# Performance work log

Hardware: AMD Instinct MI355X
Metric: run time of the kernel (lower is better)

## Reference

```python
import jax, jax.numpy as jnp
import numpy as np

N_NODES = 50000
N_EDGES = 800000
C_IN = 64
C_OUT = 64
C_MSG = C_IN + 3 + 3 + 1  # 71: feat + coords + pos-diff + dist
NUM_TYPES = 2


def setup_inputs() -> dict:
    key = jax.random.key(0)
    k0, k1, k2, k3, k4, k5 = jax.random.split(key, 6)
    input_feature = jax.random.normal(k0, (N_NODES, C_IN), dtype=jnp.float32)
    pos = jax.random.uniform(k1, (N_NODES, 3), dtype=jnp.float32)
    edge_index = jax.random.randint(k2, (2, N_EDGES), 0, N_NODES, dtype=jnp.int32)
    edge_attr = jax.random.randint(k3, (N_EDGES,), 0, NUM_TYPES, dtype=jnp.int32)
    W = jax.random.normal(k4, (NUM_TYPES, C_MSG, C_OUT), dtype=jnp.float32) / np.sqrt(C_MSG)
    b = jax.random.normal(k5, (NUM_TYPES, C_OUT), dtype=jnp.float32) * 0.01
    return {"input_feature": input_feature, "pos": pos, "W": W, "b": b,
            "edge_index": edge_index, "edge_attr": edge_attr}


def reference(input_feature, pos, W, b, edge_index, edge_attr):
    # MyConv.forward: concat node coords (graph.x[..., :3]) onto features
    x = jnp.concatenate([input_feature, pos], axis=-1)  # [N, C_IN+3]
    src = edge_index[0]  # j (source)
    dst = edge_index[1]  # i (target, aggregation index)

    x_j = x[src]                               # [E, C_IN+3]
    diff = pos[dst] - pos[src]                 # x_i[...,-3:] - x_j[...,-3:], [E, 3]
    abs_dist = jnp.linalg.norm(diff, axis=1, keepdims=True)  # [E, 1]
    msg_in = jnp.concatenate([x_j, diff, abs_dist], axis=-1)  # [E, C_MSG]

    # HeteroLinear with 2 types: compute both GEMMs, select per edge type
    y0 = msg_in @ W[0] + b[0]
    y1 = msg_in @ W[1] + b[1]
    msg = jnp.where((edge_attr == 1)[:, None], y1, y0)  # [E, C_OUT]

    # aggr='max' scatter into target nodes; empty segments -> 0 (torch_scatter fill)
    out = jax.ops.segment_max(msg, dst, num_segments=N_NODES)
    out = jnp.where(jnp.isfinite(out), out, jnp.zeros((), out.dtype))
    return out
```

## Files before the change

### kernel.cpp

```cpp
#include <hip/hip_runtime.h>
#include <math.h>

#define NNODES 50000
#define NEDGES 800000
#define COUT 64
#define TILE_E 64
#define NTILES (NEDGES / TILE_E)
#define GRID 1024
#define KEY_NEG_INF 0x007FFFFFu
#define NB1 391
#define NB1P 392
#define CHUNK 2048
#define P2CAP 2816

typedef short bf16x8 __attribute__((ext_vector_type(8)));
typedef float f32x4 __attribute__((ext_vector_type(4)));
#define MFMA16 __builtin_amdgcn_mfma_f32_16x16x32_bf16

__device__ __forceinline__ unsigned short f2bf(float x) {
    union { float f; unsigned u; } v; v.f = x;
    unsigned r = v.u + 0x7fffu + ((v.u >> 16) & 1u);
    return (unsigned short)(r >> 16);
}

__device__ __forceinline__ unsigned fkey(float v) {
    unsigned u = __float_as_uint(v);
    return u ^ ((unsigned)((int)u >> 31) | 0x80000000u);
}

__global__ void prep_kernel(const float* __restrict__ feat, unsigned short* __restrict__ featbf,
                            unsigned* __restrict__ out) {
    int i = blockIdx.x * blockDim.x + threadIdx.x;
    int st = gridDim.x * blockDim.x;
    for (int j = i; j < (NNODES * COUT) / 8; j += st) {
        const float4* pp = (const float4*)(feat + (size_t)j * 8);
        float4 x = pp[0], y = pp[1];
        union { unsigned short u[8]; uint4 v; } r;
        r.u[0] = f2bf(x.x); r.u[1] = f2bf(x.y); r.u[2] = f2bf(x.z); r.u[3] = f2bf(x.w);
        r.u[4] = f2bf(y.x); r.u[5] = f2bf(y.y); r.u[6] = f2bf(y.z); r.u[7] = f2bf(y.w);
        ((uint4*)featbf)[j] = r.v;
    }
    for (int j = i; j < NNODES * COUT; j += st) out[j] = KEY_NEG_INF;
}

__global__ __launch_bounds__(256) void p1a_kernel(const int* __restrict__ ei,
                                                  unsigned* __restrict__ cnt1) {
    __shared__ unsigned h[NB1];
    const int t = threadIdx.x, blk = blockIdx.x;
    for (int i = t; i < NB1; i += 256) h[i] = 0u;
    __syncthreads();
    const int e0 = blk * CHUNK;
    for (int i = t; i < CHUNK; i += 256) {
        int e = e0 + i;
        if (e < NEDGES) atomicAdd(&h[(unsigned)ei[NEDGES + e] >> 7], 1u);
    }
    __syncthreads();
    for (int i = t; i < NB1; i += 256) cnt1[blk * NB1P + i] = h[i];
}

__global__ __launch_bounds__(512) void p1b_kernel(const unsigned* __restrict__ cnt1,
                                                  unsigned* __restrict__ off0,
                                                  unsigned* __restrict__ totals) {
    __shared__ unsigned sh[512];
    const int t = threadIdx.x, b = blockIdx.x;
    unsigned v = (t < NB1) ? cnt1[t * NB1P + b] : 0u;
    sh[t] = v;
    __syncthreads();
    for (int off = 1; off < 512; off <<= 1) {
        unsigned add = (t >= off) ? sh[t - off] : 0u;
        __syncthreads();
        sh[t] += add;
        __syncthreads();
    }
    if (t < NB1) off0[t * NB1P + b] = sh[t] - v;
    if (t == 511) totals[b] = sh[511];
}

__global__ __launch_bounds__(512) void p1c_kernel(const unsigned* __restrict__ totals,
                                                  unsigned* __restrict__ base) {
    __shared__ unsigned sh[512];
    const int t = threadIdx.x;
    unsigned v = (t < NB1) ? totals[t] : 0u;
    sh[t] = v;
    __syncthreads();
    for (int off = 1; off < 512; off <<= 1) {
        unsigned add = (t >= off) ? sh[t - off] : 0u;
        __syncthreads();
        sh[t] += add;
        __syncthreads();
    }
    if (t <= NB1) base[t] = sh[t] - v;
}

__global__ __launch_bounds__(256) void p1d_kernel(const int* __restrict__ ei,
                                                  const int* __restrict__ ea,
                                                  const unsigned* __restrict__ off0,
                                                  const unsigned* __restrict__ base,
                                                  int2* __restrict__ rec) {
    __shared__ unsigned h[NB1];
    const int t = threadIdx.x, blk = blockIdx.x;
    for (int i = t; i < NB1; i += 256) h[i] = 0u;
    __syncthreads();
    const int e0 = blk * CHUNK;
    for (int i = t; i < CHUNK; i += 256) {
        int e = e0 + i;
        if (e < NEDGES) {
            int d = ei[NEDGES + e];
            unsigned b = (unsigned)d >> 7;
            unsigned rk = atomicAdd(&h[b], 1u);
            unsigned pos = base[b] + off0[blk * NB1P + b] + rk;
            rec[pos] = make_int2(ei[e] | (ea[e] << 20), d);
        }
    }
}

__global__ __launch_bounds__(512) void p2_kernel(const unsigned* __restrict__ base,
                                                 int2* __restrict__ rec) {
    __shared__ int2 buf[P2CAP];
    __shared__ unsigned hist[128], dbase[128];
    const int t = threadIdx.x, b = blockIdx.x;
    const unsigned lo = base[b];
    int n = (int)(base[b + 1] - lo);
    if (n > P2CAP) n = P2CAP;
    for (int i = t; i < 128; i += 512) hist[i] = 0u;
    __syncthreads();
    for (int i = t; i < n; i += 512) {
        int2 r = rec[lo + i];
        buf[i] = r;
        atomicAdd(&hist[r.y & 127], 1u);
    }
    __syncthreads();
    if (t < 64) {
        unsigned h0 = hist[2 * t], h1 = hist[2 * t + 1];
        unsigned s = h0 + h1;
        unsigned inc = s;
        #pragma unroll
        for (int off = 1; off < 64; off <<= 1) {
            unsigned nb = __shfl_up(inc, off, 64);
            if (t >= off) inc += nb;
        }
        unsigned excl = inc - s;
        dbase[2 * t] = excl;
        dbase[2 * t + 1] = excl + h0;
    }
    __syncthreads();
    for (int i = t; i < 128; i += 512) hist[i] = 0u;
    __syncthreads();
    for (int i = t; i < n; i += 512) {
        int2 r = buf[i];
        int ld = r.y & 127;
        unsigned rk = atomicAdd(&hist[ld], 1u);
        rec[lo + dbase[ld] + rk] = r;
    }
}

__global__ void finalize_kernel(float* __restrict__ out, int n) {
    int i = blockIdx.x * blockDim.x + threadIdx.x;
    int stride = gridDim.x * blockDim.x;
    for (; i < n; i += stride) {
        unsigned k = ((unsigned*)out)[i];
        unsigned u = (k & 0x80000000u) ? (k ^ 0x80000000u) : ~k;
        out[i] = (u == 0xFF800000u) ? 0.0f : __uint_as_float(u);
    }
}

__global__ __launch_bounds__(256, 4) void edge_mfma_kernel(
    const unsigned short* __restrict__ featbf, const float* __restrict__ pos,
    const float* __restrict__ W, const float* __restrict__ b,
    const int2* __restrict__ rec, unsigned* __restrict__ out)
{
    __shared__ char SMEM[37376];
    bf16x8*   Amsg = (bf16x8*)SMEM;
    unsigned* Kt   = (unsigned*)(SMEM + 20480);
    int*      dstv = (int*)(SMEM + 36864);

    const int tid = threadIdx.x;
    const int lane = tid & 63, w = tid >> 6;
    const int rg = w >> 1, cg = w & 1;
    const int la = lane & 15, lh = lane >> 4;
    const bf16x8 zero8 = {0, 0, 0, 0, 0, 0, 0, 0};

    {
        unsigned short* Ws = (unsigned short*)SMEM;
        for (int idx = tid; idx < 160 * 64; idx += 256) {
            int k = idx >> 6, j = idx & 63;
            int t = (k >= 80);
            int kk = k - t * 80;
            float v = 0.0f;
            if (kk < 71)       v = W[(t * 71 + kk) * 64 + j];
            else if (kk == 71) v = b[t * 64 + j];
            Ws[j * 160 + k] = f2bf(v);
        }
    }
    __syncthreads();
    bf16x8 wb0[5], wb1[5];
    {
        const bf16x8* Wv = (const bf16x8*)SMEM;
        const int c0 = cg * 32 + la, c1 = c0 + 16;
        #pragma unroll
        for (int ks = 0; ks < 5; ++ks) {
            wb0[ks] = Wv[c0 * 20 + ks * 4 + lh];
            wb1[ks] = Wv[c1 * 20 + ks * 4 + lh];
        }
    }
    __syncthreads();
    if (tid < 128) {
        Amsg[(9 + (tid >> 6) * 10) * 64 + (tid & 63)] = zero8;
    }
    __syncthreads();

    const int row = tid >> 2, c = tid & 3;

    int it = 0;
    for (int tile = blockIdx.x; tile < NTILES; tile += GRID, ++it) {
        const int p = it & 1;
        const int2 r2 = rec[tile * TILE_E + row];
        const int src = r2.x & 0xFFFFF;
        const int t = r2.x >> 20;
        const int ot = 1 - t;

        const uint4* g = (const uint4*)(featbf + (size_t)src * 64);
        uint4 q0 = g[2 * c], q1 = g[2 * c + 1];
        *(uint4*)&Amsg[(t * 10 + 2 * c) * 64 + row]     = q0;
        *(uint4*)&Amsg[(t * 10 + 2 * c + 1) * 64 + row] = q1;
        Amsg[(ot * 10 + 2 * c) * 64 + row]     = zero8;
        Amsg[(ot * 10 + 2 * c + 1) * 64 + row] = zero8;

        if (c == 0) {
            int dst = r2.y;
            float ps0 = pos[src * 3], ps1 = pos[src * 3 + 1], ps2 = pos[src * 3 + 2];
            float d0 = pos[dst * 3] - ps0, d1 = pos[dst * 3 + 1] - ps1, d2 = pos[dst * 3 + 2] - ps2;
            float dist = sqrtf(d0 * d0 + d1 * d1 + d2 * d2);
            union { bf16x8 v; unsigned short u[8]; } pt;
            pt.u[0] = f2bf(ps0); pt.u[1] = f2bf(ps1); pt.u[2] = f2bf(ps2);
            pt.u[3] = f2bf(d0);  pt.u[4] = f2bf(d1);  pt.u[5] = f2bf(d2);
            pt.u[6] = f2bf(dist); pt.u[7] = f2bf(1.0f);
            Amsg[(t * 10 + 8) * 64 + row] = pt.v;
        } else if (c == 1) {
            Amsg[(ot * 10 + 8) * 64 + row] = zero8;
        } else if (c == 3) {
            dstv[p * 64 + row] = r2.y;
        }
        __syncthreads();

        f32x4 acc00 = {0,0,0,0}, acc01 = {0,0,0,0}, acc10 = {0,0,0,0}, acc11 = {0,0,0,0};
        const int r0 = rg * 32 + la, r1 = r0 + 16;
        #pragma unroll
        for (int ks = 0; ks < 5; ++ks) {
            bf16x8 a0 = Amsg[(ks * 4 + lh) * 64 + r0];
            bf16x8 a1 = Amsg[(ks * 4 + lh) * 64 + r1];
            acc00 = MFMA16(a0, wb0[ks], acc00, 0, 0, 0);
            acc01 = MFMA16(a0, wb1[ks], acc01, 0, 0, 0);
            acc10 = MFMA16(a1, wb0[ks], acc10, 0, 0, 0);
            acc11 = MFMA16(a1, wb1[ks], acc11, 0, 0, 0);
        }

        const int col0 = cg * 32 + la, col1 = col0 + 16;
        #pragma unroll
        for (int i = 0; i < 4; ++i) {
            int e0 = rg * 32 + lh * 4 + i, e1 = e0 + 16;
            Kt[e0 * 64 + (col0 ^ ((e0 << 2) & 31))] = fkey(acc00[i]);
            Kt[e0 * 64 + (col1 ^ ((e0 << 2) & 31))] = fkey(acc01[i]);
            Kt[e1 * 64 + (col0 ^ ((e1 << 2) & 31))] = fkey(acc10[i]);
            Kt[e1 * 64 + (col1 ^ ((e1 << 2) & 31))] = fkey(acc11[i]);
        }
        __syncthreads();

        {
            const int colr = tid & 63;
            const int rbeg = (tid >> 6) * 16;
            unsigned cur = Kt[rbeg * 64 + (colr ^ ((rbeg << 2) & 31))];
            int curd = dstv[p * 64 + rbeg];
            #pragma unroll
            for (int r = rbeg + 1; r < rbeg + 16; ++r) {
                unsigned k = Kt[r * 64 + (colr ^ ((r << 2) & 31))];
                int d = dstv[p * 64 + r];
                if (d != curd) {
                    atomicMax(out + (size_t)curd * COUT + colr, cur);
                    curd = d; cur = k;
                } else {
                    cur = (k > cur) ? k : cur;
                }
            }
            atomicMax(out + (size_t)curd * COUT + colr, cur);
        }
    }
}

extern "C" void kernel_launch(void* const* d_in, const int* in_sizes, int n_in,
                              void* d_out, int out_size, void* d_ws, size_t ws_size,
                              hipStream_t stream) {
    const float* feat = (const float*)d_in[0];
    const float* pos  = (const float*)d_in[1];
    const float* W    = (const float*)d_in[2];
    const float* b    = (const float*)d_in[3];
    const int*   ei   = (const int*)d_in[4];
    const int*   ea   = (const int*)d_in[5];
    unsigned* out = (unsigned*)d_out;

    unsigned short* featbf = (unsigned short*)d_ws;
    int2*     rec    = (int2*)((char*)d_ws + (size_t)NNODES * COUT * 2);
    unsigned* cnt1   = (unsigned*)(rec + NEDGES);
    unsigned* off0   = cnt1 + NB1 * NB1P;
    unsigned* totals = off0 + NB1 * NB1P;
    unsigned* base   = totals + NB1P;

    prep_kernel<<<2048, 256, 0, stream>>>(feat, featbf, out);
    p1a_kernel<<<NB1, 256, 0, stream>>>(ei, cnt1);
    p1b_kernel<<<NB1, 512, 0, stream>>>(cnt1, off0, totals);
    p1c_kernel<<<1, 512, 0, stream>>>(totals, base);
    p1d_kernel<<<NB1, 256, 0, stream>>>(ei, ea, off0, base, rec);
    p2_kernel<<<NB1, 512, 0, stream>>>(base, rec);
    edge_mfma_kernel<<<GRID, 256, 0, stream>>>(featbf, pos, W, b, rec, out);
    finalize_kernel<<<2048, 256, 0, stream>>>((float*)out, NNODES * COUT);
}
```

Before: 176.4 us.

## Flush max-reduction directly from MFMA accumulators, drop LDS transpose, raise occupancy

Removes the LDS key-transpose buffer and its extra barrier. Each lane now run-length reduces its 4 accumulator rows per column pair and issues atomicMax straight from registers. This shrinks shared memory enough to raise launch bounds to 7 blocks per CU and the grid to 1792. The trade-off is more global atomics, because runs are only merged across 4 rows instead of 16. The single dstv buffer now relies on the trailing barrier before the next tile overwrites it.

```diff
diff --git a/kernel.cpp b/kernel.cpp
--- a/kernel.cpp
+++ b/kernel.cpp
@@ -6,7 +6,7 @@
 #define COUT 64
 #define TILE_E 64
 #define NTILES (NEDGES / TILE_E)
-#define GRID 1024
+#define GRID 1792
 #define KEY_NEG_INF 0x007FFFFFu
 #define NB1 391
 #define NB1P 392
@@ -164,15 +164,37 @@
     }
 }
 
-__global__ __launch_bounds__(256, 4) void edge_mfma_kernel(
+__device__ __forceinline__ void flush4x2(const f32x4& a, const f32x4& bq, int R,
+                                         const int* __restrict__ dv,
+                                         int col0, int col1,
+                                         unsigned* __restrict__ out) {
+    int curd = dv[R];
+    unsigned ca = fkey(a[0]), cb = fkey(bq[0]);
+    #pragma unroll
+    for (int j = 1; j < 4; ++j) {
+        int d = dv[R + j];
+        unsigned ka = fkey(a[j]), kb = fkey(bq[j]);
+        if (d == curd) {
+            ca = (ka > ca) ? ka : ca;
+            cb = (kb > cb) ? kb : cb;
+        } else {
+            atomicMax(out + (size_t)curd * COUT + col0, ca);
+            atomicMax(out + (size_t)curd * COUT + col1, cb);
+            curd = d; ca = ka; cb = kb;
+        }
+    }
+    atomicMax(out + (size_t)curd * COUT + col0, ca);
+    atomicMax(out + (size_t)curd * COUT + col1, cb);
+}
+
+__global__ __launch_bounds__(256, 7) void edge_mfma_kernel(
     const unsigned short* __restrict__ featbf, const float* __restrict__ pos,
     const float* __restrict__ W, const float* __restrict__ b,
     const int2* __restrict__ rec, unsigned* __restrict__ out)
 {
-    __shared__ char SMEM[37376];
-    bf16x8*   Amsg = (bf16x8*)SMEM;
-    unsigned* Kt   = (unsigned*)(SMEM + 20480);
-    int*      dstv = (int*)(SMEM + 36864);
+    __shared__ char SMEM[20736];
+    bf16x8* Amsg = (bf16x8*)SMEM;
+    int*    dstv = (int*)(SMEM + 20480);
 
     const int tid = threadIdx.x;
     const int lane = tid & 63, w = tid >> 6;
@@ -211,9 +233,7 @@
 
     const int row = tid >> 2, c = tid & 3;
 
-    int it = 0;
-    for (int tile = blockIdx.x; tile < NTILES; tile += GRID, ++it) {
-        const int p = it & 1;
+    for (int tile = blockIdx.x; tile < NTILES; tile += GRID) {
         const int2 r2 = rec[tile * TILE_E + row];
         const int src = r2.x & 0xFFFFF;
         const int t = r2.x >> 20;
@@ -239,7 +259,7 @@
         } else if (c == 1) {
             Amsg[(ot * 10 + 8) * 64 + row] = zero8;
         } else if (c == 3) {
-            dstv[p * 64 + row] = r2.y;
+            dstv[row] = r2.y;
         }
         __syncthreads();
 
@@ -255,35 +275,13 @@
             acc11 = MFMA16(a1, wb1[ks], acc11, 0, 0, 0);
         }
 
-        const int col0 = cg * 32 + la, col1 = col0 + 16;
-        #pragma unroll
-        for (int i = 0; i < 4; ++i) {
-            int e0 = rg * 32 + lh * 4 + i, e1 = e0 + 16;
-            Kt[e0 * 64 + (col0 ^ ((e0 << 2) & 31))] = fkey(acc00[i]);
-            Kt[e0 * 64 + (col1 ^ ((e0 << 2) & 31))] = fkey(acc01[i]);
-            Kt[e1 * 64 + (col0 ^ ((e1 << 2) & 31))] = fkey(acc10[i]);
-            Kt[e1 * 64 + (col1 ^ ((e1 << 2) & 31))] = fkey(acc11[i]);
-        }
-        __syncthreads();
-
         {
-            const int colr = tid & 63;
-            const int rbeg = (tid >> 6) * 16;
-            unsigned cur = Kt[rbeg * 64 + (colr ^ ((rbeg << 2) & 31))];
-            int curd = dstv[p * 64 + rbeg];
-            #pragma unroll
-            for (int r = rbeg + 1; r < rbeg + 16; ++r) {
-                unsigned k = Kt[r * 64 + (colr ^ ((r << 2) & 31))];
-                int d = dstv[p * 64 + r];
-                if (d != curd) {
-                    atomicMax(out + (size_t)curd * COUT + colr, cur);
-                    curd = d; cur = k;
-                } else {
-                    cur = (k > cur) ? k : cur;
-                }
-            }
-            atomicMax(out + (size_t)curd * COUT + colr, cur);
-        }
+            const int col0 = cg * 32 + la, col1 = col0 + 16;
+            const int R0 = rg * 32 + lh * 4;
+            flush4x2(acc00, acc01, R0,      dstv, col0, col1, out);
+            flush4x2(acc10, acc11, R0 + 16, dstv, col0, col1, out);
+        }
+        __syncthreads();
     }
 }
 
```

Result: slower. 269.6 us (+52.8%).

## Software-pipeline edge gathers across tiles and use barriers without a vmem wait

Applied to the files above, without the earlier changes.

Prefetches the next tile's edge record, source features and position values into registers while the current tile runs its MFMA and atomic scatter phases. The two __syncthreads calls are replaced by a custom barrier that waits only on LDS counters, so outstanding global loads stay in flight across barriers. The aim is to hide gather latency behind compute and atomics, at the cost of extra registers that may lower occupancy under the 4-wave launch bound.

```diff
diff --git a/kernel.cpp b/kernel.cpp
--- a/kernel.cpp
+++ b/kernel.cpp
@@ -28,6 +28,13 @@
     return u ^ ((unsigned)((int)u >> 31) | 0x80000000u);
 }
 
+__device__ __forceinline__ void soft_barrier() {
+    __builtin_amdgcn_sched_barrier(0);
+    asm volatile("s_waitcnt lgkmcnt(0)" ::: "memory");
+    __builtin_amdgcn_s_barrier();
+    __builtin_amdgcn_sched_barrier(0);
+}
+
 __global__ void prep_kernel(const float* __restrict__ feat, unsigned short* __restrict__ featbf,
                             unsigned* __restrict__ out) {
     int i = blockIdx.x * blockDim.x + threadIdx.x;
@@ -179,6 +186,21 @@
     const int rg = w >> 1, cg = w & 1;
     const int la = lane & 15, lh = lane >> 4;
     const bf16x8 zero8 = {0, 0, 0, 0, 0, 0, 0, 0};
+    const int row = tid >> 2, c = tid & 3;
+
+    int tile = blockIdx.x;
+    int2 r2 = rec[tile * TILE_E + row];
+    {
+    }
+    int src0 = r2.x & 0xFFFFF;
+    const uint4* g0 = (const uint4*)(featbf + (size_t)src0 * 64);
+    uint4 q0 = g0[2 * c], q1 = g0[2 * c + 1];
+    float cps0 = 0.f, cps1 = 0.f, cps2 = 0.f, cpd0 = 0.f, cpd1 = 0.f, cpd2 = 0.f;
+    if (c == 0) {
+        cps0 = pos[src0 * 3]; cps1 = pos[src0 * 3 + 1]; cps2 = pos[src0 * 3 + 2];
+        int d0i = r2.y;
+        cpd0 = pos[d0i * 3]; cpd1 = pos[d0i * 3 + 1]; cpd2 = pos[d0i * 3 + 2];
+    }
 
     {
         unsigned short* Ws = (unsigned short*)SMEM;
@@ -209,31 +231,22 @@
     }
     __syncthreads();
 
-    const int row = tid >> 2, c = tid & 3;
-
     int it = 0;
-    for (int tile = blockIdx.x; tile < NTILES; tile += GRID, ++it) {
+    for (; tile < NTILES; tile += GRID, ++it) {
         const int p = it & 1;
-        const int2 r2 = rec[tile * TILE_E + row];
-        const int src = r2.x & 0xFFFFF;
         const int t = r2.x >> 20;
         const int ot = 1 - t;
-
-        const uint4* g = (const uint4*)(featbf + (size_t)src * 64);
-        uint4 q0 = g[2 * c], q1 = g[2 * c + 1];
         *(uint4*)&Amsg[(t * 10 + 2 * c) * 64 + row]     = q0;
         *(uint4*)&Amsg[(t * 10 + 2 * c + 1) * 64 + row] = q1;
         Amsg[(ot * 10 + 2 * c) * 64 + row]     = zero8;
         Amsg[(ot * 10 + 2 * c + 1) * 64 + row] = zero8;
 
         if (c == 0) {
-            int dst = r2.y;
-            float ps0 = pos[src * 3], ps1 = pos[src * 3 + 1], ps2 = pos[src * 3 + 2];
-            float d0 = pos[dst * 3] - ps0, d1 = pos[dst * 3 + 1] - ps1, d2 = pos[dst * 3 + 2] - ps2;
+            float d0 = cpd0 - cps0, d1 = cpd1 - cps1, d2 = cpd2 - cps2;
             float dist = sqrtf(d0 * d0 + d1 * d1 + d2 * d2);
             union { bf16x8 v; unsigned short u[8]; } pt;
-            pt.u[0] = f2bf(ps0); pt.u[1] = f2bf(ps1); pt.u[2] = f2bf(ps2);
-            pt.u[3] = f2bf(d0);  pt.u[4] = f2bf(d1);  pt.u[5] = f2bf(d2);
+            pt.u[0] = f2bf(cps0); pt.u[1] = f2bf(cps1); pt.u[2] = f2bf(cps2);
+            pt.u[3] = f2bf(d0);   pt.u[4] = f2bf(d1);  pt.u[5] = f2bf(d2);
             pt.u[6] = f2bf(dist); pt.u[7] = f2bf(1.0f);
             Amsg[(t * 10 + 8) * 64 + row] = pt.v;
         } else if (c == 1) {
@@ -241,7 +254,12 @@
         } else if (c == 3) {
             dstv[p * 64 + row] = r2.y;
         }
-        __syncthreads();
+        soft_barrier();
+
+        const int ntile = tile + GRID;
+        const bool hasnext = (ntile < NTILES);
+        int2 nr2 = r2;
+        if (hasnext) nr2 = rec[ntile * TILE_E + row];
 
         f32x4 acc00 = {0,0,0,0}, acc01 = {0,0,0,0}, acc10 = {0,0,0,0}, acc11 = {0,0,0,0};
         const int r0 = rg * 32 + la, r1 = r0 + 16;
@@ -264,7 +282,22 @@
             Kt[e1 * 64 + (col0 ^ ((e1 << 2) & 31))] = fkey(acc10[i]);
             Kt[e1 * 64 + (col1 ^ ((e1 << 2) & 31))] = fkey(acc11[i]);
         }
-        __syncthreads();
+
+        uint4 nq0 = q0, nq1 = q1;
+        float nps0 = cps0, nps1 = cps1, nps2 = cps2;
+        float npd0 = cpd0, npd1 = cpd1, npd2 = cpd2;
+        if (hasnext) {
+            int nsrc = nr2.x & 0xFFFFF;
+            const uint4* ng = (const uint4*)(featbf + (size_t)nsrc * 64);
+            nq0 = ng[2 * c]; nq1 = ng[2 * c + 1];
+            if (c == 0) {
+                nps0 = pos[nsrc * 3]; nps1 = pos[nsrc * 3 + 1]; nps2 = pos[nsrc * 3 + 2];
+                int nd = nr2.y;
+                npd0 = pos[nd * 3]; npd1 = pos[nd * 3 + 1]; npd2 = pos[nd * 3 + 2];
+            }
+        }
+
+        soft_barrier();
 
         {
             const int colr = tid & 63;
@@ -284,6 +317,10 @@
             }
             atomicMax(out + (size_t)curd * COUT + colr, cur);
         }
+
+        r2 = nr2; q0 = nq0; q1 = nq1;
+        cps0 = nps0; cps1 = nps1; cps2 = nps2;
+        cpd0 = npd0; cpd1 = npd1; cpd2 = npd2;
     }
 }
 
```

Measured after the change: 179.7 us. About the same (+1.9%).

## Fuse prep with histogram and replace two-level scan scatter with global atomic tickets

Applied to the files above, without the earlier changes.

Merges the bf16 conversion and -inf init of the output into the per-block histogram kernel, and vectorises the init stores. Replaces the per-block offset scan and two-level base scan with a single-block column reduction plus scan that writes bucket bases and ticket counters. The scatter then claims slots with global atomics per edge. This cuts the launch count from eight to six; in exchange it adds global atomic contention on 391 counters and makes the within-bucket record order nondeterministic, which p2 re-sorts anyway.

```diff
diff --git a/kernel.cpp b/kernel.cpp
--- a/kernel.cpp
+++ b/kernel.cpp
@@ -28,11 +28,22 @@
     return u ^ ((unsigned)((int)u >> 31) | 0x80000000u);
 }
 
-__global__ void prep_kernel(const float* __restrict__ feat, unsigned short* __restrict__ featbf,
-                            unsigned* __restrict__ out) {
-    int i = blockIdx.x * blockDim.x + threadIdx.x;
-    int st = gridDim.x * blockDim.x;
-    for (int j = i; j < (NNODES * COUT) / 8; j += st) {
+__global__ __launch_bounds__(256) void k1_kernel(const float* __restrict__ feat,
+                                                 const int* __restrict__ ei,
+                                                 unsigned short* __restrict__ featbf,
+                                                 unsigned* __restrict__ out,
+                                                 unsigned* __restrict__ cnt1) {
+    __shared__ unsigned h[NB1];
+    const int t = threadIdx.x, blk = blockIdx.x;
+    for (int i = t; i < NB1; i += 256) h[i] = 0u;
+    __syncthreads();
+    const int e0 = blk * CHUNK;
+    for (int i = t; i < CHUNK; i += 256) {
+        int e = e0 + i;
+        if (e < NEDGES) atomicAdd(&h[(unsigned)ei[NEDGES + e] >> 7], 1u);
+    }
+    const int gid = blk * 256 + t, gst = NB1 * 256;
+    for (int j = gid; j < (NNODES * COUT) / 8; j += gst) {
         const float4* pp = (const float4*)(feat + (size_t)j * 8);
         float4 x = pp[0], y = pp[1];
         union { unsigned short u[8]; uint4 v; } r;
@@ -40,30 +51,21 @@
         r.u[4] = f2bf(y.x); r.u[5] = f2bf(y.y); r.u[6] = f2bf(y.z); r.u[7] = f2bf(y.w);
         ((uint4*)featbf)[j] = r.v;
     }
-    for (int j = i; j < NNODES * COUT; j += st) out[j] = KEY_NEG_INF;
-}
-
-__global__ __launch_bounds__(256) void p1a_kernel(const int* __restrict__ ei,
-                                                  unsigned* __restrict__ cnt1) {
-    __shared__ unsigned h[NB1];
-    const int t = threadIdx.x, blk = blockIdx.x;
-    for (int i = t; i < NB1; i += 256) h[i] = 0u;
-    __syncthreads();
-    const int e0 = blk * CHUNK;
-    for (int i = t; i < CHUNK; i += 256) {
-        int e = e0 + i;
-        if (e < NEDGES) atomicAdd(&h[(unsigned)ei[NEDGES + e] >> 7], 1u);
-    }
+    const uint4 ninf4 = make_uint4(KEY_NEG_INF, KEY_NEG_INF, KEY_NEG_INF, KEY_NEG_INF);
+    for (int j = gid; j < (NNODES * COUT) / 4; j += gst) ((uint4*)out)[j] = ninf4;
     __syncthreads();
     for (int i = t; i < NB1; i += 256) cnt1[blk * NB1P + i] = h[i];
 }
 
-__global__ __launch_bounds__(512) void p1b_kernel(const unsigned* __restrict__ cnt1,
-                                                  unsigned* __restrict__ off0,
-                                                  unsigned* __restrict__ totals) {
+__global__ __launch_bounds__(512) void k2_kernel(const unsigned* __restrict__ cnt1,
+                                                 unsigned* __restrict__ base,
+                                                 unsigned* __restrict__ ticket) {
     __shared__ unsigned sh[512];
-    const int t = threadIdx.x, b = blockIdx.x;
-    unsigned v = (t < NB1) ? cnt1[t * NB1P + b] : 0u;
+    const int t = threadIdx.x;
+    unsigned v = 0u;
+    if (t < NB1) {
+        for (int blk = 0; blk < NB1; ++blk) v += cnt1[blk * NB1P + t];
+    }
     sh[t] = v;
     __syncthreads();
     for (int off = 1; off < 512; off <<= 1) {
@@ -72,45 +74,21 @@
         sh[t] += add;
         __syncthreads();
     }
-    if (t < NB1) off0[t * NB1P + b] = sh[t] - v;
-    if (t == 511) totals[b] = sh[511];
-}
-
-__global__ __launch_bounds__(512) void p1c_kernel(const unsigned* __restrict__ totals,
-                                                  unsigned* __restrict__ base) {
-    __shared__ unsigned sh[512];
-    const int t = threadIdx.x;
-    unsigned v = (t < NB1) ? totals[t] : 0u;
-    sh[t] = v;
-    __syncthreads();
-    for (int off = 1; off < 512; off <<= 1) {
-        unsigned add = (t >= off) ? sh[t - off] : 0u;
-        __syncthreads();
-        sh[t] += add;
-        __syncthreads();
-    }
-    if (t <= NB1) base[t] = sh[t] - v;
-}
-
-__global__ __launch_bounds__(256) void p1d_kernel(const int* __restrict__ ei,
-                                                  const int* __restrict__ ea,
-                                                  const unsigned* __restrict__ off0,
-                                                  const unsigned* __restrict__ base,
-                                                  int2* __restrict__ rec) {
-    __shared__ unsigned h[NB1];
-    const int t = threadIdx.x, blk = blockIdx.x;
-    for (int i = t; i < NB1; i += 256) h[i] = 0u;
-    __syncthreads();
-    const int e0 = blk * CHUNK;
-    for (int i = t; i < CHUNK; i += 256) {
-        int e = e0 + i;
-        if (e < NEDGES) {
-            int d = ei[NEDGES + e];
-            unsigned b = (unsigned)d >> 7;
-            unsigned rk = atomicAdd(&h[b], 1u);
-            unsigned pos = base[b] + off0[blk * NB1P + b] + rk;
-            rec[pos] = make_int2(ei[e] | (ea[e] << 20), d);
-        }
+    if (t <= NB1) {
+        unsigned excl = sh[t] - v;
+        base[t] = excl;
+        if (t < NB1) ticket[t] = excl;
+    }
+}
+
+__global__ void k3_kernel(const int* __restrict__ ei, const int* __restrict__ ea,
+                          unsigned* __restrict__ ticket, int2* __restrict__ rec) {
+    int i = blockIdx.x * blockDim.x + threadIdx.x;
+    int st = gridDim.x * blockDim.x;
+    for (int e = i; e < NEDGES; e += st) {
+        int d = ei[NEDGES + e];
+        unsigned p = atomicAdd(&ticket[(unsigned)d >> 7], 1u);
+        rec[p] = make_int2(ei[e] | (ea[e] << 20), d);
     }
 }
 
@@ -301,15 +279,12 @@
     unsigned short* featbf = (unsigned short*)d_ws;
     int2*     rec    = (int2*)((char*)d_ws + (size_t)NNODES * COUT * 2);
     unsigned* cnt1   = (unsigned*)(rec + NEDGES);
-    unsigned* off0   = cnt1 + NB1 * NB1P;
-    unsigned* totals = off0 + NB1 * NB1P;
-    unsigned* base   = totals + NB1P;
-
-    prep_kernel<<<2048, 256, 0, stream>>>(feat, featbf, out);
-    p1a_kernel<<<NB1, 256, 0, stream>>>(ei, cnt1);
-    p1b_kernel<<<NB1, 512, 0, stream>>>(cnt1, off0, totals);
-    p1c_kernel<<<1, 512, 0, stream>>>(totals, base);
-    p1d_kernel<<<NB1, 256, 0, stream>>>(ei, ea, off0, base, rec);
+    unsigned* base   = cnt1 + NB1 * NB1P;
+    unsigned* ticket = base + (NB1 + 1);
+
+    k1_kernel<<<NB1, 256, 0, stream>>>(feat, ei, featbf, out, cnt1);
+    k2_kernel<<<1, 512, 0, stream>>>(cnt1, base, ticket);
+    k3_kernel<<<2048, 256, 0, stream>>>(ei, ea, ticket, rec);
     p2_kernel<<<NB1, 512, 0, stream>>>(base, rec);
     edge_mfma_kernel<<<GRID, 256, 0, stream>>>(featbf, pos, W, b, rec, out);
     finalize_kernel<<<2048, 256, 0, stream>>>((float*)out, NNODES * COUT);
```

Result: slower. 457.6 us (+159.4%).
